# Performance work log

Measured on AMD Instinct MI355X. Metric: run time of the kernel, lower is better.

Reference implementation:

```python
import jax, jax.numpy as jnp
import numpy as np

N_PATCHES = 14
N_BLOCKS = 12
HIDDEN = 768
N_HEADS = 12
D_HEAD = HIDDEN // N_HEADS
MLP_RATIO = 4
OUT_D = 1000
BATCH = 32
C, H, W = 3, 224, 224
PS = H // N_PATCHES            # 16
INPUT_D = C * PS * PS          # 768
SEQ = N_PATCHES ** 2 + 1       # 197
LN_EPS = 1e-5


def _pos_emb(length, d):
    i = np.arange(length, dtype=np.float64)[:, None]
    j = np.arange(d, dtype=np.float64)[None, :]
    angle = i / (10000.0 ** ((j - (j % 2)) / d))
    pe = np.where(j % 2 == 0, np.sin(angle), np.cos(angle))
    return jnp.asarray(pe, dtype=jnp.float32)  # [length, d]


def setup_inputs() -> dict:
    key = jax.random.key(0)
    ks = jax.random.split(key, 16)
    s = 0.02
    inp = {
        "x": jax.random.normal(ks[0], (BATCH, C, H, W), jnp.float32),
        "W_map": jax.random.normal(ks[1], (INPUT_D, HIDDEN), jnp.float32) * s,
        "b_map": jnp.zeros((HIDDEN,), jnp.float32),
        "cls_tok": jax.random.uniform(ks[2], (1, HIDDEN), jnp.float32),
        "pos_emb": _pos_emb(SEQ, HIDDEN),
        "ln1_s": jnp.ones((N_BLOCKS, HIDDEN), jnp.float32),
        "ln1_b": jnp.zeros((N_BLOCKS, HIDDEN), jnp.float32),
        "Wq": jax.random.normal(ks[3], (N_BLOCKS, N_HEADS, D_HEAD, D_HEAD), jnp.float32) * s,
        "bq": jnp.zeros((N_BLOCKS, N_HEADS, D_HEAD), jnp.float32),
        "Wk": jax.random.normal(ks[4], (N_BLOCKS, N_HEADS, D_HEAD, D_HEAD), jnp.float32) * s,
        "bk": jnp.zeros((N_BLOCKS, N_HEADS, D_HEAD), jnp.float32),
        "Wv": jax.random.normal(ks[5], (N_BLOCKS, N_HEADS, D_HEAD, D_HEAD), jnp.float32) * s,
        "bv": jnp.zeros((N_BLOCKS, N_HEADS, D_HEAD), jnp.float32),
        "ln2_s": jnp.ones((N_BLOCKS, HIDDEN), jnp.float32),
        "ln2_b": jnp.zeros((N_BLOCKS, HIDDEN), jnp.float32),
        "W1": jax.random.normal(ks[6], (N_BLOCKS, HIDDEN, MLP_RATIO * HIDDEN), jnp.float32) * s,
        "b1": jnp.zeros((N_BLOCKS, MLP_RATIO * HIDDEN), jnp.float32),
        "W2": jax.random.normal(ks[7], (N_BLOCKS, MLP_RATIO * HIDDEN, HIDDEN), jnp.float32) * s,
        "b2": jnp.zeros((N_BLOCKS, HIDDEN), jnp.float32),
        "W_out": jax.random.normal(ks[8], (HIDDEN, OUT_D), jnp.float32) * s,
        "b_out": jnp.zeros((OUT_D,), jnp.float32),
    }
    return inp


def _layernorm(x, scale, bias):
    m = jnp.mean(x, axis=-1, keepdims=True)
    v = jnp.mean(jnp.square(x - m), axis=-1, keepdims=True)
    return (x - m) * jax.lax.rsqrt(v + LN_EPS) * scale + bias


def _patchify(x):
    # [N,C,H,W] -> [N, np*np, C*ps*ps], channel-major flatten per patch (matches torch flatten)
    n = x.shape[0]
    p = x.reshape(n, C, N_PATCHES, PS, N_PATCHES, PS)
    p = p.transpose(0, 2, 4, 1, 3, 5)  # [N, np, np, C, ps, ps]
    return p.reshape(n, N_PATCHES * N_PATCHES, INPUT_D)


def _msa(x, Wq, bq, Wk, bk, Wv, bv):
    # x: [N,S,D]; per-head separate linears, faithful scale = 1/sqrt(n_heads)
    n, s_, _ = x.shape
    xh = x.reshape(n, s_, N_HEADS, D_HEAD)
    q = jnp.einsum('nshd,hde->nhse', xh, Wq) + bq[None, :, None, :]
    k = jnp.einsum('nshd,hde->nhse', xh, Wk) + bk[None, :, None, :]
    v = jnp.einsum('nshd,hde->nhse', xh, Wv) + bv[None, :, None, :]
    scale = 1.0 / jnp.sqrt(jnp.float32(N_HEADS))
    att = jax.nn.softmax(jnp.einsum('nhse,nhte->nhst', q, k) * scale, axis=-1)
    o = jnp.einsum('nhst,nhte->nhse', att, v)
    return o.transpose(0, 2, 1, 3).reshape(n, s_, HIDDEN)


def reference(x, W_map, b_map, cls_tok, pos_emb, ln1_s, ln1_b, Wq, bq, Wk, bk, Wv, bv,
              ln2_s, ln2_b, W1, b1, W2, b2, W_out, b_out):
    n = x.shape[0]
    tokens = _patchify(x) @ W_map + b_map                       # [N, np^2, D]
    tokens = jnp.concatenate([jnp.broadcast_to(cls_tok[None], (n, 1, HIDDEN)), tokens], axis=1)
    h = tokens + pos_emb[None]                                  # [N, S, D]
    for blk in range(N_BLOCKS):
        attn_out = _msa(_layernorm(h, ln1_s[blk], ln1_b[blk]),
                        Wq[blk], bq[blk], Wk[blk], bk[blk], Wv[blk], bv[blk])
        out = h + attn_out
        # faithful to source: MLP branch reads norm2(x), not norm2(out)
        m = _layernorm(h, ln2_s[blk], ln2_b[blk])
        m = jax.nn.gelu(m @ W1[blk] + b1[blk], approximate=False) @ W2[blk] + b2[blk]
        h = out + m
    cls = h[:, 0]                                               # [N, D]
    return jax.nn.softmax(cls @ W_out + b_out, axis=1)          # [N, out_d]
```

## Files before the change

kernel.cpp:

```cpp
#include <hip/hip_runtime.h>
#include <math.h>

#define BATCH   32
#define SEQ     197
#define HIDDEN  768
#define NHEADS  12
#define DHEAD   64
#define NBLOCKS 12
#define MLP_D   3072
#define OUTD    1000
#define NPATCH  196
#define M_TOK   (BATCH*SEQ)
#define M_PAD   6400
#define LN_EPS  1e-5f
#define SP      208

typedef _Float16 f16;
typedef _Float16 f16x8 __attribute__((ext_vector_type(8)));
typedef _Float16 f16x4 __attribute__((ext_vector_type(4)));
typedef float    f32x4 __attribute__((ext_vector_type(4)));

__device__ __forceinline__ float gelu_exact(float x) {
    return 0.5f * x * (1.0f + erff(x * 0.70710678118654752f));
}

__device__ __forceinline__ void gload_lds16(const void* g, void* l) {
    __builtin_amdgcn_global_load_lds(
        (const __attribute__((address_space(1))) void*)g,
        (__attribute__((address_space(3))) void*)l, 16, 0, 0);
}

__device__ __forceinline__ f16x8 lds_ld(const char* base, int row, int rs, int kbyte) {
    return *(const f16x8*)(base + row*rs + (kbyte ^ ((row & 7) << 4)));
}

__global__ __launch_bounds__(256) void patchify_kernel(const float* __restrict__ x,
                                                       f16* __restrict__ patches) {
    int row = blockIdx.x;
    int n = row / NPATCH;
    int p = row % NPATCH;
    int pi = p / 14, pj = p % 14;
    for (int k = threadIdx.x; k < 768; k += 256) {
        int c   = k >> 8;
        int r   = (k >> 4) & 15;
        int col = k & 15;
        patches[(size_t)row*768 + k] =
            (f16)x[(((size_t)n*3 + c)*224 + (pi*16 + r))*224 + pj*16 + col];
    }
}

__global__ __launch_bounds__(256) void convtrans_kernel(const float* __restrict__ in,
                                                        f16* __restrict__ out,
                                                        int R, int C) {
    __shared__ float tile[32][33];
    int r0 = blockIdx.y * 32, c0 = blockIdx.x * 32;
    int tx = threadIdx.x & 31, ty = threadIdx.x >> 5;
    #pragma unroll
    for (int i = 0; i < 4; ++i) {
        int r = ty + i*8;
        tile[r][tx] = in[(size_t)(r0 + r)*C + c0 + tx];
    }
    __syncthreads();
    #pragma unroll
    for (int i = 0; i < 4; ++i) {
        int r = ty + i*8;
        out[(size_t)(c0 + r)*R + r0 + tx] = (f16)tile[tx][r];
    }
}

__global__ __launch_bounds__(256) void qkvtrans_kernel(const float* __restrict__ Wq,
                                                       const float* __restrict__ Wk,
                                                       const float* __restrict__ Wv,
                                                       f16* __restrict__ outT) {
    int b = blockIdx.x;
    int blkL = b / 36, rem = b % 36;
    int hh = rem / 3, mat = rem % 3;
    const float* in = (mat == 0 ? Wq : mat == 1 ? Wk : Wv) + ((size_t)(blkL*12 + hh))*4096;
    f16* out = outT + (size_t)b * 4096;
    __shared__ float tile[64][65];
    int t = threadIdx.x;
    for (int i = t; i < 4096; i += 256) tile[i >> 6][i & 63] = in[i];
    __syncthreads();
    for (int i = t; i < 4096; i += 256) out[i] = (f16)tile[i & 63][i >> 6];
}

__global__ __launch_bounds__(256) void assemble_kernel(const float* __restrict__ tokens,
                                                       const float* __restrict__ cls,
                                                       const float* __restrict__ pos,
                                                       float* __restrict__ h) {
    int r = blockIdx.x;
    int n = r / SEQ, s = r % SEQ;
    for (int c = threadIdx.x; c < 768; c += 256) {
        float v = (s == 0) ? cls[c] : tokens[(size_t)(n*NPATCH + s - 1)*768 + c];
        h[(size_t)r*768 + c] = v + pos[s*768 + c];
    }
}

template<typename OT>
__global__ __launch_bounds__(256) void layernorm_kernel(const float* __restrict__ x,
                                                        const float* __restrict__ scale,
                                                        const float* __restrict__ bias,
                                                        OT* __restrict__ out) {
    int r = blockIdx.x;
    int t = threadIdx.x;
    const float* xr = x + (size_t)r*768;
    float v0 = xr[t], v1 = xr[t+256], v2 = xr[t+512];
    float s = v0 + v1 + v2;
    #pragma unroll
    for (int off = 32; off > 0; off >>= 1) s += __shfl_xor(s, off);
    __shared__ float red[4];
    int wid = t >> 6, lane = t & 63;
    if (lane == 0) red[wid] = s;
    __syncthreads();
    float mean = (red[0]+red[1]+red[2]+red[3]) * (1.0f/768.0f);
    __syncthreads();
    float d0 = v0-mean, d1 = v1-mean, d2 = v2-mean;
    float q = d0*d0 + d1*d1 + d2*d2;
    #pragma unroll
    for (int off = 32; off > 0; off >>= 1) q += __shfl_xor(q, off);
    if (lane == 0) red[wid] = q;
    __syncthreads();
    float var = (red[0]+red[1]+red[2]+red[3]) * (1.0f/768.0f);
    float inv = rsqrtf(var + LN_EPS);
    OT* orow = out + (size_t)r*768;
    orow[t]     = (OT)(d0*inv*scale[t]     + bias[t]);
    orow[t+256] = (OT)(d1*inv*scale[t+256] + bias[t+256]);
    orow[t+512] = (OT)(d2*inv*scale[t+512] + bias[t+512]);
}

__global__ __launch_bounds__(256) void fused_attn_kernel(
        const f16* __restrict__ lnh, const f16* __restrict__ qkvT,
        const float* __restrict__ bq, const float* __restrict__ bk,
        const float* __restrict__ bv, float* __restrict__ O) {
    int n = blockIdx.x, h = blockIdx.y;
    int t = threadIdx.x, wid = t >> 6, lane = t & 63;
    int lr = lane & 15;
    int lg = lane >> 4;

    __shared__ char lds[145408];
    char* Xs  = lds;
    char* Qs  = lds + 26624;
    char* Ks  = lds + 53248;
    char* VsT = lds + 79872;
    char* Ws  = lds + 112640;
    char* Ps  = lds + 112640 + wid*8192;

    const char* xsrc = (const char*)(lnh + (size_t)n*SEQ*768 + h*64);
    for (int c = t; c < SP*8; c += 256) {
        int s = c >> 3, kb = (c & 7) * 16;
        f16x8 v = {};
        if (s < SEQ) v = *(const f16x8*)(xsrc + (size_t)s*1536 + kb);
        *(f16x8*)(Xs + s*128 + (kb ^ ((s & 7) << 4))) = v;
    }
    const char* wsrc = (const char*)(qkvT) + (size_t)h * 3 * 4096 * 2;
    for (int c = t; c < 1536; c += 256) {
        int byte = c * 16, row = byte >> 7, kb = byte & 127;
        f16x8 v = *(const f16x8*)(wsrc + byte);
        *(f16x8*)(Ws + row*128 + (kb ^ ((row & 7) << 4))) = v;
    }
    for (int c = t; c < 384; c += 256) {
        int e = c / 6, sl = c % 6;
        int kb = 416 + sl * 16;
        *(f16x8*)(VsT + e*512 + (kb ^ ((e & 7) << 4))) = (f16x8){};
    }
    __syncthreads();

    for (int idx = wid; idx < 39; idx += 4) {
        int mat = idx / 13, mt = idx % 13;
        const float* bias = (mat == 0) ? bq : (mat == 1) ? bk : bv;
        #pragma unroll
        for (int nt = 0; nt < 4; ++nt) {
            f32x4 acc = {};
            #pragma unroll
            for (int ks = 0; ks < 2; ++ks) {
                f16x8 a = lds_ld(Xs, mt*16 + lr, 128, lg*16 + ks*64);
                f16x8 b = lds_ld(Ws, mat*64 + nt*16 + lr, 128, lg*16 + ks*64);
                acc = __builtin_amdgcn_mfma_f32_16x16x32_f16(a, b, acc, 0, 0, 0);
            }
            float bb = bias[h*64 + nt*16 + lr];
            if (mat < 2) {
                char* dst = (mat == 0) ? Qs : Ks;
                #pragma unroll
                for (int j = 0; j < 4; ++j) {
                    int s = mt*16 + lg*4 + j;
                    int eb = (nt*16 + lr) * 2;
                    *(f16*)(dst + s*128 + (eb ^ ((s & 7) << 4))) = (f16)(acc[j] + bb);
                }
            } else {
                int e = nt*16 + lr;
                int sb = (mt*16 + lg*4) * 2;
                f16x4 pv;
                #pragma unroll
                for (int j = 0; j < 4; ++j) pv[j] = (f16)(acc[j] + bb);
                *(f16x4*)(VsT + e*512 + (sb ^ ((e & 7) << 4))) = pv;
            }
        }
    }
    __syncthreads();

    for (int c = lane; c < 96; c += 64) {
        int r = c / 6, kb = 416 + (c % 6) * 16;
        *(f16x8*)(Ps + r*512 + (kb ^ ((r & 7) << 4))) = (f16x8){};
    }

    const float scale = 0.28867513459481288f;
    for (int mt = wid; mt < 13; mt += 4) {
        f32x4 sacc[13];
        #pragma unroll
        for (int nt = 0; nt < 13; ++nt) sacc[nt] = (f32x4){};
        #pragma unroll
        for (int ks = 0; ks < 2; ++ks) {
            f16x8 a = lds_ld(Qs, mt*16 + lr, 128, lg*16 + ks*64);
            #pragma unroll
            for (int nt = 0; nt < 13; ++nt) {
                f16x8 b = lds_ld(Ks, nt*16 + lr, 128, lg*16 + ks*64);
                sacc[nt] = __builtin_amdgcn_mfma_f32_16x16x32_f16(a, b, sacc[nt], 0, 0, 0);
            }
        }
        float mx0 = -1e30f, mx1 = -1e30f, mx2 = -1e30f, mx3 = -1e30f;
        #pragma unroll
        for (int nt = 0; nt < 13; ++nt) {
            bool valid = (nt*16 + lr) < SEQ;
            #pragma unroll
            for (int j = 0; j < 4; ++j) {
                float v = valid ? sacc[nt][j] * scale : -1e30f;
                sacc[nt][j] = v;
            }
            mx0 = fmaxf(mx0, sacc[nt][0]); mx1 = fmaxf(mx1, sacc[nt][1]);
            mx2 = fmaxf(mx2, sacc[nt][2]); mx3 = fmaxf(mx3, sacc[nt][3]);
        }
        #pragma unroll
        for (int off = 1; off < 16; off <<= 1) {
            mx0 = fmaxf(mx0, __shfl_xor(mx0, off));
            mx1 = fmaxf(mx1, __shfl_xor(mx1, off));
            mx2 = fmaxf(mx2, __shfl_xor(mx2, off));
            mx3 = fmaxf(mx3, __shfl_xor(mx3, off));
        }
        float s0 = 0.f, s1 = 0.f, s2 = 0.f, s3 = 0.f;
        #pragma unroll
        for (int nt = 0; nt < 13; ++nt) {
            float p0 = expf(sacc[nt][0] - mx0); sacc[nt][0] = p0; s0 += p0;
            float p1 = expf(sacc[nt][1] - mx1); sacc[nt][1] = p1; s1 += p1;
            float p2 = expf(sacc[nt][2] - mx2); sacc[nt][2] = p2; s2 += p2;
            float p3 = expf(sacc[nt][3] - mx3); sacc[nt][3] = p3; s3 += p3;
        }
        #pragma unroll
        for (int off = 1; off < 16; off <<= 1) {
            s0 += __shfl_xor(s0, off); s1 += __shfl_xor(s1, off);
            s2 += __shfl_xor(s2, off); s3 += __shfl_xor(s3, off);
        }
        float i0 = 1.0f/s0, i1 = 1.0f/s1, i2 = 1.0f/s2, i3 = 1.0f/s3;
        #pragma unroll
        for (int nt = 0; nt < 13; ++nt) {
            int cb = (nt*16 + lr) * 2;
            { int r = lg*4 + 0; *(f16*)(Ps + r*512 + (cb ^ ((r & 7) << 4))) = (f16)(sacc[nt][0] * i0); }
            { int r = lg*4 + 1; *(f16*)(Ps + r*512 + (cb ^ ((r & 7) << 4))) = (f16)(sacc[nt][1] * i1); }
            { int r = lg*4 + 2; *(f16*)(Ps + r*512 + (cb ^ ((r & 7) << 4))) = (f16)(sacc[nt][2] * i2); }
            { int r = lg*4 + 3; *(f16*)(Ps + r*512 + (cb ^ ((r & 7) << 4))) = (f16)(sacc[nt][3] * i3); }
        }
        f32x4 oacc[4] = {};
        #pragma unroll
        for (int ks = 0; ks < 8; ++ks) {
            f16x8 a = lds_ld(Ps, lr, 512, lg*16 + ks*64);
            #pragma unroll
            for (int nt = 0; nt < 4; ++nt) {
                f16x8 b = lds_ld(VsT, nt*16 + lr, 512, lg*16 + ks*64);
                oacc[nt] = __builtin_amdgcn_mfma_f32_16x16x32_f16(a, b, oacc[nt], 0, 0, 0);
            }
        }
        #pragma unroll
        for (int nt = 0; nt < 4; ++nt) {
            #pragma unroll
            for (int j = 0; j < 4; ++j) {
                int s = mt*16 + lg*4 + j;
                if (s < SEQ)
                    O[((size_t)(n*SEQ + s))*768 + h*64 + nt*16 + lr] = oacc[nt][j];
            }
        }
    }
}

template<int MODE, int TN>
__global__ __launch_bounds__(256) void hgemm_kernel(
        const f16* __restrict__ A,
        const f16* __restrict__ BT,
        const float* __restrict__ bias,
        const float* __restrict__ res1,
        const float* __restrict__ res2,
        void* __restrict__ Cout, int M, int N, int K, int nbx) {
    constexpr int BISS = TN / 32;
    constexpr int WN   = TN / 2;
    __shared__ f16 As[2][128*64];
    __shared__ f16 Bs[2][TN*64];
    int t = threadIdx.x;
    int wid = t >> 6, lane = t & 63;
    int lr = lane & 15, lg = lane >> 4;
    int wr = wid >> 1, wc = wid & 1;

    int nwg = gridDim.x, bid = blockIdx.x;
    int q = nwg >> 3, r = nwg & 7;
    int xcd = bid & 7, idx = bid >> 3;
    int swz = (xcd < r) ? xcd*(q+1) + idx : r*(q+1) + (xcd-r)*q + idx;
    int bn = (swz % nbx) * TN;
    int bm = (swz / nbx) * 128;

    int arow[4], aswk[4], brow[BISS], bswk[BISS];
    #pragma unroll
    for (int i = 0; i < 4; ++i) {
        int fb = i*4096 + wid*1024 + lane*16;
        int row = fb >> 7, slot = (fb >> 4) & 7;
        arow[i] = row; aswk[i] = (slot ^ (row & 7)) * 8;
    }
    #pragma unroll
    for (int i = 0; i < BISS; ++i) {
        int fb = i*4096 + wid*1024 + lane*16;
        int row = fb >> 7, slot = (fb >> 4) & 7;
        brow[i] = row; bswk[i] = (slot ^ (row & 7)) * 8;
    }

    #define STAGE(P, K0)                                                          \
        do {                                                                      \
            _Pragma("unroll")                                                     \
            for (int i = 0; i < 4; ++i)                                           \
                gload_lds16(A + (size_t)(bm + arow[i])*K + (K0) + aswk[i],        \
                            (char*)&As[P][0] + i*4096 + wid*1024);                \
            _Pragma("unroll")                                                     \
            for (int i = 0; i < BISS; ++i)                                        \
                gload_lds16(BT + (size_t)(bn + brow[i])*K + (K0) + bswk[i],       \
                            (char*)&Bs[P][0] + i*4096 + wid*1024);                \
        } while (0)

    f32x4 acc[4][BISS] = {};
    int nk = K >> 6;

    STAGE(0, 0);
    __syncthreads();
    for (int kt = 0; kt < nk; ++kt) {
        int cur = kt & 1;
        if (kt + 1 < nk) STAGE(cur ^ 1, (kt + 1) * 64);
        const char* Ab = (const char*)&As[cur][0];
        const char* Bb = (const char*)&Bs[cur][0];
        #pragma unroll
        for (int ks = 0; ks < 2; ++ks) {
            f16x8 a[4], b[BISS];
            #pragma unroll
            for (int m = 0; m < 4; ++m)
                a[m] = lds_ld(Ab, wr*64 + m*16 + lr, 128, lg*16 + ks*64);
            #pragma unroll
            for (int nn = 0; nn < BISS; ++nn)
                b[nn] = lds_ld(Bb, wc*WN + nn*16 + lr, 128, lg*16 + ks*64);
            #pragma unroll
            for (int m = 0; m < 4; ++m)
                #pragma unroll
                for (int nn = 0; nn < BISS; ++nn)
                    acc[m][nn] = __builtin_amdgcn_mfma_f32_16x16x32_f16(a[m], b[nn], acc[m][nn], 0, 0, 0);
        }
        __syncthreads();
    }
    #undef STAGE

    int row0 = bm + wr*64 + lg*4;
    int col0 = bn + wc*WN + lr;
    #pragma unroll
    for (int m = 0; m < 4; ++m) {
        #pragma unroll
        for (int nn = 0; nn < BISS; ++nn) {
            int col = col0 + nn*16;
            float bv = bias[col];
            #pragma unroll
            for (int j = 0; j < 4; ++j) {
                int row = row0 + m*16 + j;
                if (row >= M) continue;
                float v = acc[m][nn][j] + bv;
                size_t idx = (size_t)row*N + col;
                if (MODE == 0) {
                    if (res1) v += res1[idx] + res2[idx];
                    ((float*)Cout)[idx] = v;
                } else {
                    ((f16*)Cout)[idx] = (f16)gelu_exact(v);
                }
            }
        }
    }
}

__global__ __launch_bounds__(256) void head_kernel(const float* __restrict__ h,
                                                   const float* __restrict__ W_out,
                                                   const float* __restrict__ b_out,
                                                   float* __restrict__ out) {
    int n = blockIdx.x, t = threadIdx.x;
    __shared__ float xs[HIDDEN];
    __shared__ float red[4];
    const float* hr = h + (size_t)n*SEQ*HIDDEN;
    for (int k = t; k < HIDDEN; k += 256) xs[k] = hr[k];
    __syncthreads();

    bool v3 = t < (OUTD - 768);
    int c3 = v3 ? (t + 768) : t;
    float a0 = 0.f, a1 = 0.f, a2 = 0.f, a3 = 0.f;
    #pragma unroll 8
    for (int k = 0; k < HIDDEN; ++k) {
        float xv = xs[k];
        const float* wr = W_out + (size_t)k*OUTD;
        a0 = fmaf(xv, wr[t],       a0);
        a1 = fmaf(xv, wr[t + 256], a1);
        a2 = fmaf(xv, wr[t + 512], a2);
        a3 = fmaf(xv, wr[c3],      a3);
    }
    a0 += b_out[t]; a1 += b_out[t + 256]; a2 += b_out[t + 512];
    a3 = v3 ? (a3 + b_out[t + 768]) : -1e30f;

    int wid = t >> 6, lane = t & 63;
    float mx = fmaxf(fmaxf(a0, a1), fmaxf(a2, a3));
    #pragma unroll
    for (int off = 32; off > 0; off >>= 1) mx = fmaxf(mx, __shfl_xor(mx, off));
    if (lane == 0) red[wid] = mx;
    __syncthreads();
    mx = fmaxf(fmaxf(red[0], red[1]), fmaxf(red[2], red[3]));
    __syncthreads();

    float p0 = expf(a0 - mx), p1 = expf(a1 - mx), p2 = expf(a2 - mx);
    float p3 = v3 ? expf(a3 - mx) : 0.f;
    float s = p0 + p1 + p2 + p3;
    #pragma unroll
    for (int off = 32; off > 0; off >>= 1) s += __shfl_xor(s, off);
    if (lane == 0) red[wid] = s;
    __syncthreads();
    s = red[0] + red[1] + red[2] + red[3];
    float inv = 1.0f / s;

    float* orow = out + (size_t)n*OUTD;
    orow[t]       = p0 * inv;
    orow[t + 256] = p1 * inv;
    orow[t + 512] = p2 * inv;
    if (v3) orow[t + 768] = p3 * inv;
}

extern "C" void kernel_launch(void* const* d_in, const int* in_sizes, int n_in,
                              void* d_out, int out_size, void* d_ws, size_t ws_size,
                              hipStream_t stream) {
    const float* x     = (const float*)d_in[0];
    const float* W_map = (const float*)d_in[1];
    const float* b_map = (const float*)d_in[2];
    const float* cls_t = (const float*)d_in[3];
    const float* pos   = (const float*)d_in[4];
    const float* ln1_s = (const float*)d_in[5];
    const float* ln1_b = (const float*)d_in[6];
    const float* Wq    = (const float*)d_in[7];
    const float* bq    = (const float*)d_in[8];
    const float* Wk    = (const float*)d_in[9];
    const float* bk    = (const float*)d_in[10];
    const float* Wv    = (const float*)d_in[11];
    const float* bv    = (const float*)d_in[12];
    const float* ln2_s = (const float*)d_in[13];
    const float* ln2_b = (const float*)d_in[14];
    const float* W1    = (const float*)d_in[15];
    const float* b1    = (const float*)d_in[16];
    const float* W2    = (const float*)d_in[17];
    const float* b2    = (const float*)d_in[18];
    const float* W_out = (const float*)d_in[19];
    const float* b_out = (const float*)d_in[20];
    float* out = (float*)d_out;

    char* w = (char*)d_ws;
    const size_t SZ32 = (size_t)M_TOK * HIDDEN * 4;
    float* h        = (float*)w;  w += SZ32;
    float* attn_out = (float*)w;  w += SZ32;
    f16*   mid_h    = (f16*)w;    w += (size_t)M_PAD * MLP_D * 2;
    f16*   lnh      = (f16*)w;    w += (size_t)M_PAD * HIDDEN * 2;
    f16*   W1T      = (f16*)w;    w += (size_t)MLP_D * HIDDEN * 2;
    f16*   W2T      = (f16*)w;    w += (size_t)HIDDEN * MLP_D * 2;
    f16*   WmapT    = (f16*)w;    w += (size_t)768 * 768 * 2;
    f16*   qkvT     = (f16*)w;    w += (size_t)NBLOCKS * NHEADS * 3 * 64 * 64 * 2;

    f16* patches_h = mid_h;
    patchify_kernel<<<BATCH*NPATCH, 256, 0, stream>>>(x, patches_h);
    {
        dim3 g(768/32, 768/32);
        convtrans_kernel<<<g, 256, 0, stream>>>(W_map, WmapT, 768, 768);
    }
    qkvtrans_kernel<<<NBLOCKS*NHEADS*3, 256, 0, stream>>>(Wq, Wk, Wv, qkvT);
    hgemm_kernel<0,64><<<49*12, 256, 0, stream>>>(patches_h, WmapT, b_map,
                                                  nullptr, nullptr,
                                                  (void*)attn_out, BATCH*NPATCH, 768, 768, 12);
    assemble_kernel<<<M_TOK, 256, 0, stream>>>(attn_out, cls_t, pos, h);

    for (int blk = 0; blk < NBLOCKS; ++blk) {
        layernorm_kernel<f16><<<M_TOK, 256, 0, stream>>>(h, ln1_s + blk*768, ln1_b + blk*768, lnh);
        {
            dim3 g(BATCH, NHEADS);
            fused_attn_kernel<<<g, 256, 0, stream>>>(lnh,
                qkvT + (size_t)blk*NHEADS*3*4096,
                bq + (size_t)blk*768, bk + (size_t)blk*768, bv + (size_t)blk*768,
                attn_out);
        }
        layernorm_kernel<f16><<<M_TOK, 256, 0, stream>>>(h, ln2_s + blk*768, ln2_b + blk*768, lnh);
        {
            dim3 g(MLP_D/32, HIDDEN/32);
            convtrans_kernel<<<g, 256, 0, stream>>>(W1 + (size_t)blk*HIDDEN*MLP_D, W1T, HIDDEN, MLP_D);
        }
        hgemm_kernel<1,128><<<50*24, 256, 0, stream>>>(lnh, W1T, b1 + (size_t)blk*MLP_D,
                                                       nullptr, nullptr,
                                                       (void*)mid_h, M_TOK, MLP_D, 768, 24);
        {
            dim3 g(HIDDEN/32, MLP_D/32);
            convtrans_kernel<<<g, 256, 0, stream>>>(W2 + (size_t)blk*MLP_D*HIDDEN, W2T, MLP_D, HIDDEN);
        }
        hgemm_kernel<0,64><<<50*12, 256, 0, stream>>>(mid_h, W2T, b2 + (size_t)blk*HIDDEN,
                                                      h, attn_out,
                                                      (void*)h, M_TOK, HIDDEN, MLP_D, 12);
    }

    head_kernel<<<BATCH, 256, 0, stream>>>(h, W_out, b_out, out);
}
```

Baseline: 2.807 ms.

## Fuse dual layernorms and weight transposes; use 64-wide tiles for MLP GEMM

Computes both layernorms (ln1 and ln2) of the residual stream in one kernel writing two fp16 outputs, so h is read once and one launch is saved per block. Merges the W1 and W2 fp32-to-fp16 transposes into a single launch using a z-dimension. Removes the TN template from the GEMM, so the W1 GEMM now uses 128x64 tiles with twice as many workgroups instead of 128x128. The narrower tile raises occupancy and parallelism but lowers arithmetic intensity and increases A-tile reloads.

```diff
diff --git a/kernel.cpp b/kernel.cpp
--- a/kernel.cpp
+++ b/kernel.cpp
@@ -68,6 +68,33 @@
     }
 }
 
+__global__ __launch_bounds__(256) void convtrans2_kernel(const float* __restrict__ W1,
+                                                         const float* __restrict__ W2,
+                                                         f16* __restrict__ W1T,
+                                                         f16* __restrict__ W2T) {
+    int z = blockIdx.z;
+    const float* in = z ? W2 : W1;
+    f16* out = z ? W2T : W1T;
+    int R = z ? MLP_D : HIDDEN;
+    int C = z ? HIDDEN : MLP_D;
+    int bx = z ? blockIdx.y : blockIdx.x;
+    int by = z ? blockIdx.x : blockIdx.y;
+    __shared__ float tile[32][33];
+    int r0 = by * 32, c0 = bx * 32;
+    int tx = threadIdx.x & 31, ty = threadIdx.x >> 5;
+    #pragma unroll
+    for (int i = 0; i < 4; ++i) {
+        int r = ty + i*8;
+        tile[r][tx] = in[(size_t)(r0 + r)*C + c0 + tx];
+    }
+    __syncthreads();
+    #pragma unroll
+    for (int i = 0; i < 4; ++i) {
+        int r = ty + i*8;
+        out[(size_t)(c0 + r)*R + r0 + tx] = (f16)tile[tx][r];
+    }
+}
+
 __global__ __launch_bounds__(256) void qkvtrans_kernel(const float* __restrict__ Wq,
                                                        const float* __restrict__ Wk,
                                                        const float* __restrict__ Wv,
@@ -96,11 +123,13 @@
     }
 }
 
-template<typename OT>
-__global__ __launch_bounds__(256) void layernorm_kernel(const float* __restrict__ x,
-                                                        const float* __restrict__ scale,
-                                                        const float* __restrict__ bias,
-                                                        OT* __restrict__ out) {
+__global__ __launch_bounds__(256) void layernorm2_kernel(const float* __restrict__ x,
+                                                         const float* __restrict__ s1,
+                                                         const float* __restrict__ b1,
+                                                         const float* __restrict__ s2,
+                                                         const float* __restrict__ b2,
+                                                         f16* __restrict__ o1,
+                                                         f16* __restrict__ o2) {
     int r = blockIdx.x;
     int t = threadIdx.x;
     const float* xr = x + (size_t)r*768;
@@ -122,10 +151,15 @@
     __syncthreads();
     float var = (red[0]+red[1]+red[2]+red[3]) * (1.0f/768.0f);
     float inv = rsqrtf(var + LN_EPS);
-    OT* orow = out + (size_t)r*768;
-    orow[t]     = (OT)(d0*inv*scale[t]     + bias[t]);
-    orow[t+256] = (OT)(d1*inv*scale[t+256] + bias[t+256]);
-    orow[t+512] = (OT)(d2*inv*scale[t+512] + bias[t+512]);
+    d0 *= inv; d1 *= inv; d2 *= inv;
+    f16* p1 = o1 + (size_t)r*768;
+    f16* p2 = o2 + (size_t)r*768;
+    p1[t]     = (f16)(d0*s1[t]     + b1[t]);
+    p1[t+256] = (f16)(d1*s1[t+256] + b1[t+256]);
+    p1[t+512] = (f16)(d2*s1[t+512] + b1[t+512]);
+    p2[t]     = (f16)(d0*s2[t]     + b2[t]);
+    p2[t+256] = (f16)(d1*s2[t+256] + b2[t+256]);
+    p2[t+512] = (f16)(d2*s2[t+512] + b2[t+512]);
 }
 
 __global__ __launch_bounds__(256) void fused_attn_kernel(
@@ -280,7 +314,7 @@
     }
 }
 
-template<int MODE, int TN>
+template<int MODE>
 __global__ __launch_bounds__(256) void hgemm_kernel(
         const f16* __restrict__ A,
         const f16* __restrict__ BT,
@@ -288,10 +322,8 @@
         const float* __restrict__ res1,
         const float* __restrict__ res2,
         void* __restrict__ Cout, int M, int N, int K, int nbx) {
-    constexpr int BISS = TN / 32;
-    constexpr int WN   = TN / 2;
     __shared__ f16 As[2][128*64];
-    __shared__ f16 Bs[2][TN*64];
+    __shared__ f16 Bs[2][64*64];
     int t = threadIdx.x;
     int wid = t >> 6, lane = t & 63;
     int lr = lane & 15, lg = lane >> 4;
@@ -301,21 +333,15 @@
     int q = nwg >> 3, r = nwg & 7;
     int xcd = bid & 7, idx = bid >> 3;
     int swz = (xcd < r) ? xcd*(q+1) + idx : r*(q+1) + (xcd-r)*q + idx;
-    int bn = (swz % nbx) * TN;
+    int bn = (swz % nbx) * 64;
     int bm = (swz / nbx) * 128;
 
-    int arow[4], aswk[4], brow[BISS], bswk[BISS];
+    int arow[4], aswk[4];
     #pragma unroll
     for (int i = 0; i < 4; ++i) {
         int fb = i*4096 + wid*1024 + lane*16;
         int row = fb >> 7, slot = (fb >> 4) & 7;
         arow[i] = row; aswk[i] = (slot ^ (row & 7)) * 8;
-    }
-    #pragma unroll
-    for (int i = 0; i < BISS; ++i) {
-        int fb = i*4096 + wid*1024 + lane*16;
-        int row = fb >> 7, slot = (fb >> 4) & 7;
-        brow[i] = row; bswk[i] = (slot ^ (row & 7)) * 8;
     }
 
     #define STAGE(P, K0)                                                          \
@@ -325,12 +351,12 @@
                 gload_lds16(A + (size_t)(bm + arow[i])*K + (K0) + aswk[i],        \
                             (char*)&As[P][0] + i*4096 + wid*1024);                \
             _Pragma("unroll")                                                     \
-            for (int i = 0; i < BISS; ++i)                                        \
-                gload_lds16(BT + (size_t)(bn + brow[i])*K + (K0) + bswk[i],       \
+            for (int i = 0; i < 2; ++i)                                           \
+                gload_lds16(BT + (size_t)(bn + arow[i])*K + (K0) + aswk[i],       \
                             (char*)&Bs[P][0] + i*4096 + wid*1024);                \
         } while (0)
 
-    f32x4 acc[4][BISS] = {};
+    f32x4 acc[4][2] = {};
     int nk = K >> 6;
 
     STAGE(0, 0);
@@ -342,17 +368,17 @@
         const char* Bb = (const char*)&Bs[cur][0];
         #pragma unroll
         for (int ks = 0; ks < 2; ++ks) {
-            f16x8 a[4], b[BISS];
+            f16x8 a[4], b[2];
             #pragma unroll
             for (int m = 0; m < 4; ++m)
                 a[m] = lds_ld(Ab, wr*64 + m*16 + lr, 128, lg*16 + ks*64);
             #pragma unroll
-            for (int nn = 0; nn < BISS; ++nn)
-                b[nn] = lds_ld(Bb, wc*WN + nn*16 + lr, 128, lg*16 + ks*64);
+            for (int nn = 0; nn < 2; ++nn)
+                b[nn] = lds_ld(Bb, wc*32 + nn*16 + lr, 128, lg*16 + ks*64);
             #pragma unroll
             for (int m = 0; m < 4; ++m)
                 #pragma unroll
-                for (int nn = 0; nn < BISS; ++nn)
+                for (int nn = 0; nn < 2; ++nn)
                     acc[m][nn] = __builtin_amdgcn_mfma_f32_16x16x32_f16(a[m], b[nn], acc[m][nn], 0, 0, 0);
         }
         __syncthreads();
@@ -360,11 +386,11 @@
     #undef STAGE
 
     int row0 = bm + wr*64 + lg*4;
-    int col0 = bn + wc*WN + lr;
+    int col0 = bn + wc*32 + lr;
     #pragma unroll
     for (int m = 0; m < 4; ++m) {
         #pragma unroll
-        for (int nn = 0; nn < BISS; ++nn) {
+        for (int nn = 0; nn < 2; ++nn) {
             int col = col0 + nn*16;
             float bv = bias[col];
             #pragma unroll
@@ -467,7 +493,8 @@
     float* h        = (float*)w;  w += SZ32;
     float* attn_out = (float*)w;  w += SZ32;
     f16*   mid_h    = (f16*)w;    w += (size_t)M_PAD * MLP_D * 2;
-    f16*   lnh      = (f16*)w;    w += (size_t)M_PAD * HIDDEN * 2;
+    f16*   lnh1     = (f16*)w;    w += (size_t)M_PAD * HIDDEN * 2;
+    f16*   lnh2     = (f16*)w;    w += (size_t)M_PAD * HIDDEN * 2;
     f16*   W1T      = (f16*)w;    w += (size_t)MLP_D * HIDDEN * 2;
     f16*   W2T      = (f16*)w;    w += (size_t)HIDDEN * MLP_D * 2;
     f16*   WmapT    = (f16*)w;    w += (size_t)768 * 768 * 2;
@@ -480,35 +507,33 @@
         convtrans_kernel<<<g, 256, 0, stream>>>(W_map, WmapT, 768, 768);
     }
     qkvtrans_kernel<<<NBLOCKS*NHEADS*3, 256, 0, stream>>>(Wq, Wk, Wv, qkvT);
-    hgemm_kernel<0,64><<<49*12, 256, 0, stream>>>(patches_h, WmapT, b_map,
-                                                  nullptr, nullptr,
-                                                  (void*)attn_out, BATCH*NPATCH, 768, 768, 12);
+    hgemm_kernel<0><<<49*12, 256, 0, stream>>>(patches_h, WmapT, b_map,
+                                               nullptr, nullptr,
+                                               (void*)attn_out, BATCH*NPATCH, 768, 768, 12);
     assemble_kernel<<<M_TOK, 256, 0, stream>>>(attn_out, cls_t, pos, h);
 
     for (int blk = 0; blk < NBLOCKS; ++blk) {
-        layernorm_kernel<f16><<<M_TOK, 256, 0, stream>>>(h, ln1_s + blk*768, ln1_b + blk*768, lnh);
+        layernorm2_kernel<<<M_TOK, 256, 0, stream>>>(h,
+            ln1_s + blk*768, ln1_b + blk*768, ln2_s + blk*768, ln2_b + blk*768,
+            lnh1, lnh2);
+        {
+            dim3 g(MLP_D/32, HIDDEN/32, 2);
+            convtrans2_kernel<<<g, 256, 0, stream>>>(W1 + (size_t)blk*HIDDEN*MLP_D,
+                                                     W2 + (size_t)blk*MLP_D*HIDDEN, W1T, W2T);
+        }
         {
             dim3 g(BATCH, NHEADS);
-            fused_attn_kernel<<<g, 256, 0, stream>>>(lnh,
+            fused_attn_kernel<<<g, 256, 0, stream>>>(lnh1,
                 qkvT + (size_t)blk*NHEADS*3*4096,
                 bq + (size_t)blk*768, bk + (size_t)blk*768, bv + (size_t)blk*768,
                 attn_out);
         }
-        layernorm_kernel<f16><<<M_TOK, 256, 0, stream>>>(h, ln2_s + blk*768, ln2_b + blk*768, lnh);
-        {
-            dim3 g(MLP_D/32, HIDDEN/32);
-            convtrans_kernel<<<g, 256, 0, stream>>>(W1 + (size_t)blk*HIDDEN*MLP_D, W1T, HIDDEN, MLP_D);
-        }
-        hgemm_kernel<1,128><<<50*24, 256, 0, stream>>>(lnh, W1T, b1 + (size_t)blk*MLP_D,
-                                                       nullptr, nullptr,
-                                                       (void*)mid_h, M_TOK, MLP_D, 768, 24);
-        {
-            dim3 g(HIDDEN/32, MLP_D/32);
-            convtrans_kernel<<<g, 256, 0, stream>>>(W2 + (size_t)blk*MLP_D*HIDDEN, W2T, MLP_D, HIDDEN);
-        }
-        hgemm_kernel<0,64><<<50*12, 256, 0, stream>>>(mid_h, W2T, b2 + (size_t)blk*HIDDEN,
-                                                      h, attn_out,
-                                                      (void*)h, M_TOK, HIDDEN, MLP_D, 12);
+        hgemm_kernel<1><<<50*48, 256, 0, stream>>>(lnh2, W1T, b1 + (size_t)blk*MLP_D,
+                                                   nullptr, nullptr,
+                                                   (void*)mid_h, M_TOK, MLP_D, 768, 48);
+        hgemm_kernel<0><<<50*12, 256, 0, stream>>>(mid_h, W2T, b2 + (size_t)blk*HIDDEN,
+                                                   h, attn_out,
+                                                   (void*)h, M_TOK, HIDDEN, MLP_D, 12);
     }
 
     head_kernel<<<BATCH, 256, 0, stream>>>(h, W_out, b_out, out);
```

After: 2.704 ms. 1.04x faster.
